# Kernel tuning notes

Hardware: AMD Instinct MI355X
Metric: run time of the kernel (lower is better)

Reference implementation:

```python
import jax, jax.numpy as jnp
import numpy as np

N, E = 50000, 800000
IN_DIM, HID, OUT, HEADS = 128, 128, 64, 4
C1 = HID // HEADS  # 32 per-head channels in gat1
NEG_SLOPE = 0.2


def _gat_conv(x, src, dst, W, a_src, a_dst, b, heads, ch):
    """PyG GATConv (inference): gather -> edge attention -> segment softmax -> scatter."""
    n = x.shape[0]
    h = (x @ W).reshape(n, heads, ch)                      # [N,H,C]
    alpha_src = jnp.einsum('nhc,hc->nh', h, a_src)         # [N,H]
    alpha_dst = jnp.einsum('nhc,hc->nh', h, a_dst)         # [N,H]
    e = jax.nn.leaky_relu(alpha_src[src] + alpha_dst[dst], NEG_SLOPE)  # [E,H]
    m = jax.ops.segment_max(e, dst, num_segments=n)        # per-target max (stable softmax)
    e = jnp.exp(e - m[dst])
    denom = jax.ops.segment_sum(e, dst, num_segments=n)
    alpha = e / (denom[dst] + 1e-16)                       # [E,H]
    out = jax.ops.segment_sum(h[src] * alpha[:, :, None], dst, num_segments=n)  # [N,H,C]
    return out.reshape(n, heads * ch) + b


def setup_inputs() -> dict:
    key = jax.random.key(0)
    ks = jax.random.split(key, 16)
    x = jax.random.normal(ks[0], (N, IN_DIM), dtype=jnp.float32)
    edge_index = jax.random.randint(ks[1], (2, E), 0, N, dtype=jnp.int64)
    s = lambda fan_in: 1.0 / np.sqrt(fan_in)
    return {
        'x': x,
        'edge_index': edge_index,
        'W1': jax.random.normal(ks[2], (IN_DIM, HEADS * C1), jnp.float32) * s(IN_DIM),
        'a_src1': jax.random.normal(ks[3], (HEADS, C1), jnp.float32) * s(C1),
        'a_dst1': jax.random.normal(ks[4], (HEADS, C1), jnp.float32) * s(C1),
        'b1': jnp.zeros((HID,), jnp.float32),
        'W2': jax.random.normal(ks[5], (HID, OUT), jnp.float32) * s(HID),
        'a_src2': jax.random.normal(ks[6], (1, OUT), jnp.float32) * s(OUT),
        'a_dst2': jax.random.normal(ks[7], (1, OUT), jnp.float32) * s(OUT),
        'b2': jnp.zeros((OUT,), jnp.float32),
        'pw1': jax.random.normal(ks[8], (OUT, OUT), jnp.float32) * s(OUT),
        'pb1': jnp.zeros((OUT,), jnp.float32),
        'pw2': jax.random.normal(ks[9], (OUT, OUT), jnp.float32) * s(OUT),
        'pb2': jnp.zeros((OUT,), jnp.float32),
    }


def reference(x, edge_index, W1, a_src1, a_dst1, b1, W2, a_src2, a_dst2, b2, pw1, pb1, pw2, pb2):
    n = x.shape[0]
    # PyG GATConv add_self_loops=True
    loops = jnp.arange(n, dtype=edge_index.dtype)
    src = jnp.concatenate([edge_index[0], loops])
    dst = jnp.concatenate([edge_index[1], loops])
    h = jax.nn.elu(_gat_conv(x, src, dst, W1, a_src1, a_dst1, b1, HEADS, C1))
    h = jax.nn.elu(_gat_conv(h, src, dst, W2, a_src2, a_dst2, b2, 1, OUT))
    # origin_proj: Linear -> ReLU -> Linear
    h = jax.nn.relu(h @ pw1 + pb1)
    return h @ pw2 + pb2
```

## Files before the change

kernel.cpp:

```cpp
#include <hip/hip_runtime.h>
#include <math.h>

#define N_NODES 50000
#define N_EDGES 800000
#define ET (N_EDGES + N_NODES)
#define IN_DIM 128
#define HID 128
#define OUT_DIM 64
#define BW 64
#define NBUCK ((N_NODES + BW - 1) / BW)
#define NBLK 256
#define EPB 3328

typedef __attribute__((ext_vector_type(8))) short bf16x8;
typedef __attribute__((ext_vector_type(4))) float f32x4;

__device__ __forceinline__ float lrelu(float x){ return x >= 0.f ? x : 0.2f * x; }
__device__ __forceinline__ float eluf(float x){ return x > 0.f ? x : expm1f(x); }
__device__ __forceinline__ unsigned f2bf(float f){
    unsigned u = __float_as_uint(f);
    return (u + 0x7fffu + ((u >> 16) & 1u)) >> 16;
}
__device__ __forceinline__ float bflo(unsigned u){ return __uint_as_float(u << 16); }
__device__ __forceinline__ float bfhi(unsigned u){ return __uint_as_float(u & 0xffff0000u); }

__global__ __launch_bounds__(256) void k_count(const int* __restrict__ dst, int* __restrict__ C)
{
    __shared__ int cnt[NBUCK];
    const int tid = threadIdx.x, blk = blockIdx.x;
    for (int i = tid; i < NBUCK; i += 256) cnt[i] = 0;
    __syncthreads();
    #pragma unroll
    for (int j = 0; j < EPB / 256; j++) {
        const int e = blk * EPB + j * 256 + tid;
        if (e < ET) {
            const int d = (e < N_EDGES) ? dst[e] : (e - N_EDGES);
            atomicAdd(&cnt[d >> 6], 1);
        }
    }
    __syncthreads();
    for (int b = tid; b < NBUCK; b += 256) C[b * NBLK + blk] = cnt[b];
}

__global__ __launch_bounds__(256) void k_bsumA(const int* __restrict__ C, int* __restrict__ bsum2)
{
    __shared__ int red[4];
    int v = C[blockIdx.x * NBLK + threadIdx.x];
    #pragma unroll
    for (int off = 32; off > 0; off >>= 1) v += __shfl_down(v, off);
    if ((threadIdx.x & 63) == 0) red[threadIdx.x >> 6] = v;
    __syncthreads();
    if (threadIdx.x == 0) bsum2[blockIdx.x] = red[0] + red[1] + red[2] + red[3];
}

__global__ __launch_bounds__(1024) void k_bscanB(const int* __restrict__ bsum2, int* __restrict__ boff2)
{
    __shared__ int part[1024];
    const int t = threadIdx.x;
    int v = (t < NBUCK) ? bsum2[t] : 0;
    part[t] = v;
    __syncthreads();
    #pragma unroll
    for (int d = 1; d < 1024; d <<= 1) {
        int add = (t >= d) ? part[t - d] : 0;
        __syncthreads();
        part[t] += add;
        __syncthreads();
    }
    if (t < NBUCK) boff2[t] = part[t] - v;
    if (t == 0) boff2[NBUCK] = ET;
}

__global__ __launch_bounds__(256) void k_cscanC(const int* __restrict__ C,
                                                const int* __restrict__ boff2,
                                                int* __restrict__ Cs)
{
    __shared__ int part[256];
    const int t = threadIdx.x, b = blockIdx.x;
    int v = C[b * NBLK + t];
    part[t] = v;
    __syncthreads();
    #pragma unroll
    for (int d = 1; d < 256; d <<= 1) {
        int add = (t >= d) ? part[t - d] : 0;
        __syncthreads();
        part[t] += add;
        __syncthreads();
    }
    Cs[b * NBLK + t] = boff2[b] + part[t] - v;
}

__global__ __launch_bounds__(256) void k_part2(const int* __restrict__ src,
                                               const int* __restrict__ dst,
                                               const int* __restrict__ Cs,
                                               uint2* __restrict__ part)
{
    __shared__ int base[NBUCK];
    __shared__ int cnt[NBUCK];
    const int tid = threadIdx.x, blk = blockIdx.x;
    for (int b = tid; b < NBUCK; b += 256) { base[b] = Cs[b * NBLK + blk]; cnt[b] = 0; }
    __syncthreads();
    #pragma unroll
    for (int j = 0; j < EPB / 256; j++) {
        const int e = blk * EPB + j * 256 + tid;
        if (e < ET) {
            int s, d;
            if (e < N_EDGES) { s = src[e]; d = dst[e]; } else { s = d = e - N_EDGES; }
            const int b = d >> 6;
            const int r = atomicAdd(&cnt[b], 1);
            part[base[b] + r] = make_uint2((unsigned)d, (unsigned)s);
        }
    }
}

__global__ __launch_bounds__(256) void k_scat2(const int* __restrict__ boff2,
                                               const uint2* __restrict__ part,
                                               int* __restrict__ rowptr,
                                               int* __restrict__ csr_src)
{
    __shared__ int cnt64[BW];
    __shared__ int nbase[BW];
    const int b = blockIdx.x, tid = threadIdx.x;
    const int n0 = b * BW;
    const int lo = boff2[b], hi = boff2[b + 1];
    if (tid < BW) cnt64[tid] = 0;
    __syncthreads();
    for (int i = lo + tid; i < hi; i += 256) {
        atomicAdd(&cnt64[part[i].x & (BW - 1)], 1);
    }
    __syncthreads();
    if (tid < BW) {
        int v = cnt64[tid];
        int incl = v;
        #pragma unroll
        for (int off = 1; off < 64; off <<= 1) {
            int t2 = __shfl_up(incl, off);
            if (tid >= off) incl += t2;
        }
        const int excl = incl - v;
        nbase[tid] = excl;
        const int n = n0 + tid;
        if (n < N_NODES) rowptr[n] = lo + excl;
        cnt64[tid] = 0;
    }
    if (b == 0 && tid == 0) rowptr[N_NODES] = ET;
    __syncthreads();
    for (int i = lo + tid; i < hi; i += 256) {
        const uint2 p = part[i];
        const int dn = (int)p.x & (BW - 1);
        const int r = atomicAdd(&cnt64[dn], 1);
        csr_src[lo + nbase[dn] + r] = (int)p.y;
    }
}

__global__ __launch_bounds__(256, 2) void k_gemm1(
    const float* __restrict__ x, const float* __restrict__ W1,
    const float* __restrict__ a_s, const float* __restrict__ a_d,
    unsigned* __restrict__ h1b, float* __restrict__ as1, float* __restrict__ ad1)
{
    __shared__ unsigned sWt[128 * 68];
    __shared__ unsigned sxb[64 * 68];
    const int tid = threadIdx.x;
    const int wave = tid >> 6;
    const int lane = tid & 63;
    const int ll   = lane & 15;
    const int quad = lane >> 4;
    const int n0 = blockIdx.x * 64;

    for (int idx = tid; idx < 8192; idx += 256) {
        const int n = idx & 127, kp = idx >> 7;
        const float w0 = W1[(2 * kp) * 128 + n];
        const float w1 = W1[(2 * kp + 1) * 128 + n];
        sWt[n * 68 + kp] = f2bf(w0) | (f2bf(w1) << 16);
    }
    for (int idx = tid; idx < 4096; idx += 256) {
        const int node = idx >> 6, kp = idx & 63;
        const int n = n0 + node;
        unsigned pk = 0;
        if (n < N_NODES) {
            const float x0 = x[n * 128 + 2 * kp];
            const float x1 = x[n * 128 + 2 * kp + 1];
            pk = f2bf(x0) | (f2bf(x1) << 16);
        }
        sxb[node * 68 + kp] = pk;
    }
    __syncthreads();

    f32x4 acc[8];
    #pragma unroll
    for (int t = 0; t < 8; t++) acc[t] = (f32x4){0.f, 0.f, 0.f, 0.f};

    #pragma unroll
    for (int kk = 0; kk < 4; kk++) {
        const int kpo = 16 * kk + 4 * quad;
        const bf16x8 a = *(const bf16x8*)&sxb[(16 * wave + ll) * 68 + kpo];
        #pragma unroll
        for (int t = 0; t < 8; t++) {
            const bf16x8 b = *(const bf16x8*)&sWt[(16 * t + ll) * 68 + kpo];
            acc[t] = __builtin_amdgcn_mfma_f32_16x16x32_bf16(a, b, acc[t], 0, 0, 0);
        }
    }

    float as_v[8], ad_v[8];
    #pragma unroll
    for (int t = 0; t < 8; t++) { as_v[t] = a_s[16 * t + ll]; ad_v[t] = a_d[16 * t + ll]; }
    unsigned short* h1u = (unsigned short*)h1b;
    #pragma unroll
    for (int r = 0; r < 4; r++) {
        const int n = n0 + 16 * wave + 4 * quad + r;
        float ps0 = acc[0][r] * as_v[0] + acc[1][r] * as_v[1];
        float ps1 = acc[2][r] * as_v[2] + acc[3][r] * as_v[3];
        float ps2 = acc[4][r] * as_v[4] + acc[5][r] * as_v[5];
        float ps3 = acc[6][r] * as_v[6] + acc[7][r] * as_v[7];
        float pd0 = acc[0][r] * ad_v[0] + acc[1][r] * ad_v[1];
        float pd1 = acc[2][r] * ad_v[2] + acc[3][r] * ad_v[3];
        float pd2 = acc[4][r] * ad_v[4] + acc[5][r] * ad_v[5];
        float pd3 = acc[6][r] * ad_v[6] + acc[7][r] * ad_v[7];
        #pragma unroll
        for (int off = 1; off < 16; off <<= 1) {
            ps0 += __shfl_xor(ps0, off); ps1 += __shfl_xor(ps1, off);
            ps2 += __shfl_xor(ps2, off); ps3 += __shfl_xor(ps3, off);
            pd0 += __shfl_xor(pd0, off); pd1 += __shfl_xor(pd1, off);
            pd2 += __shfl_xor(pd2, off); pd3 += __shfl_xor(pd3, off);
        }
        if (n < N_NODES) {
            #pragma unroll
            for (int t = 0; t < 8; t++)
                h1u[n * 128 + 16 * t + ll] = (unsigned short)f2bf(acc[t][r]);
            if (ll == 0) {
                as1[n * 4 + 0] = ps0; as1[n * 4 + 1] = ps1;
                as1[n * 4 + 2] = ps2; as1[n * 4 + 3] = ps3;
                ad1[n * 4 + 0] = pd0; ad1[n * 4 + 1] = pd1;
                ad1[n * 4 + 2] = pd2; ad1[n * 4 + 3] = pd3;
            }
        }
    }
}

__global__ __launch_bounds__(256) void k_aggr1(
    const int* __restrict__ rowptr, const int* __restrict__ csr_src,
    const float* __restrict__ as1, const float* __restrict__ ad1,
    const uint4* __restrict__ h1u4, float* __restrict__ acc1)
{
    const int d  = blockIdx.x * 16 + (threadIdx.x >> 4);
    const int c8 = threadIdx.x & 15;
    const int hd = c8 >> 2;
    const int r0 = rowptr[d], r1 = rowptr[d + 1];
    const float adv = ad1[d * 4 + hd];
    float den = 0.f;
    float acc[8];
    #pragma unroll
    for (int m = 0; m < 8; m++) acc[m] = 0.f;
    int i = r0;
    for (; i + 2 <= r1; i += 2) {
        const int s0 = csr_src[i], s1 = csr_src[i + 1];
        const float e0 = as1[s0 * 4 + hd], e1 = as1[s1 * 4 + hd];
        const uint4 u0 = h1u4[s0 * 16 + c8];
        const uint4 u1 = h1u4[s1 * 16 + c8];
        const float w0 = expf(lrelu(e0 + adv));
        const float w1 = expf(lrelu(e1 + adv));
        den += w0 + w1;
        acc[0] = fmaf(bflo(u0.x), w0, acc[0]); acc[1] = fmaf(bfhi(u0.x), w0, acc[1]);
        acc[2] = fmaf(bflo(u0.y), w0, acc[2]); acc[3] = fmaf(bfhi(u0.y), w0, acc[3]);
        acc[4] = fmaf(bflo(u0.z), w0, acc[4]); acc[5] = fmaf(bfhi(u0.z), w0, acc[5]);
        acc[6] = fmaf(bflo(u0.w), w0, acc[6]); acc[7] = fmaf(bfhi(u0.w), w0, acc[7]);
        acc[0] = fmaf(bflo(u1.x), w1, acc[0]); acc[1] = fmaf(bfhi(u1.x), w1, acc[1]);
        acc[2] = fmaf(bflo(u1.y), w1, acc[2]); acc[3] = fmaf(bfhi(u1.y), w1, acc[3]);
        acc[4] = fmaf(bflo(u1.z), w1, acc[4]); acc[5] = fmaf(bfhi(u1.z), w1, acc[5]);
        acc[6] = fmaf(bflo(u1.w), w1, acc[6]); acc[7] = fmaf(bfhi(u1.w), w1, acc[7]);
    }
    if (i < r1) {
        const int s = csr_src[i];
        const float w = expf(lrelu(as1[s * 4 + hd] + adv));
        const uint4 u = h1u4[s * 16 + c8];
        den += w;
        acc[0] = fmaf(bflo(u.x), w, acc[0]); acc[1] = fmaf(bfhi(u.x), w, acc[1]);
        acc[2] = fmaf(bflo(u.y), w, acc[2]); acc[3] = fmaf(bfhi(u.y), w, acc[3]);
        acc[4] = fmaf(bflo(u.z), w, acc[4]); acc[5] = fmaf(bfhi(u.z), w, acc[5]);
        acc[6] = fmaf(bflo(u.w), w, acc[6]); acc[7] = fmaf(bfhi(u.w), w, acc[7]);
    }
    const float inv = 1.f / (den + 1e-16f);
    float4 o0 = make_float4(acc[0] * inv, acc[1] * inv, acc[2] * inv, acc[3] * inv);
    float4 o1 = make_float4(acc[4] * inv, acc[5] * inv, acc[6] * inv, acc[7] * inv);
    ((float4*)acc1)[d * 32 + 2 * c8 + 0] = o0;
    ((float4*)acc1)[d * 32 + 2 * c8 + 1] = o1;
}

__global__ __launch_bounds__(256, 4) void k_layer2(
    const float* __restrict__ acc1, const float* __restrict__ b1,
    const float* __restrict__ W2, const float* __restrict__ a_s2, const float* __restrict__ a_d2,
    unsigned* __restrict__ h2b, float* __restrict__ as2, float* __restrict__ ad2)
{
    __shared__ float sW[32 * 64];
    __shared__ float sx[128 * 32];
    float4* sW4 = (float4*)sW;
    float4* sx4 = (float4*)sx;
    const float4* a14 = (const float4*)acc1;
    const float4* W24 = (const float4*)W2;
    const float4* b14 = (const float4*)b1;
    const int tid = threadIdx.x;
    const int cg = tid & 7;
    const int ng = tid >> 3;
    const int n0 = blockIdx.x * 128;

    float4 acc[4][2];
    #pragma unroll
    for (int m = 0; m < 4; m++) { acc[m][0] = make_float4(0,0,0,0); acc[m][1] = make_float4(0,0,0,0); }

    for (int c = 0; c < 4; c++) {
        __syncthreads();
        #pragma unroll
        for (int j = 0; j < 2; j++) {
            const int idx = tid + 256 * j;
            float4 v = W24[c * 512 + idx];
            const int k = idx >> 4, f = idx & 15;
            sW4[k * 16 + ((f & 1) << 3) + (f >> 1)] = v;
        }
        #pragma unroll
        for (int j = 0; j < 4; j++) {
            const int idx = tid + 256 * j;
            const int node = idx >> 3, q = idx & 7;
            const int n = n0 + node;
            float4 v = make_float4(0,0,0,0);
            if (n < N_NODES) {
                v = a14[n * 32 + c * 8 + q];
                const float4 bb = b14[c * 8 + q];
                v.x = eluf(v.x + bb.x);
                v.y = eluf(v.y + bb.y);
                v.z = eluf(v.z + bb.z);
                v.w = eluf(v.w + bb.w);
            }
            sx4[node * 8 + (q ^ ((node >> 3) & 7))] = v;
        }
        __syncthreads();
        #pragma unroll 2
        for (int k4 = 0; k4 < 8; k4++) {
            float4 w0[4], w1[4];
            #pragma unroll
            for (int ks = 0; ks < 4; ks++) {
                w0[ks] = sW4[(4 * k4 + ks) * 16 + cg];
                w1[ks] = sW4[(4 * k4 + ks) * 16 + 8 + cg];
            }
            float4 xv[4];
            #pragma unroll
            for (int m = 0; m < 4; m++) {
                const int node = 4 * ng + m;
                xv[m] = sx4[node * 8 + (k4 ^ ((node >> 3) & 7))];
            }
            #pragma unroll
            for (int m = 0; m < 4; m++) {
                const float4 xm = xv[m];
                #define FMA8(S, KS) \
                    acc[m][0].x = fmaf(S, w0[KS].x, acc[m][0].x); \
                    acc[m][0].y = fmaf(S, w0[KS].y, acc[m][0].y); \
                    acc[m][0].z = fmaf(S, w0[KS].z, acc[m][0].z); \
                    acc[m][0].w = fmaf(S, w0[KS].w, acc[m][0].w); \
                    acc[m][1].x = fmaf(S, w1[KS].x, acc[m][1].x); \
                    acc[m][1].y = fmaf(S, w1[KS].y, acc[m][1].y); \
                    acc[m][1].z = fmaf(S, w1[KS].z, acc[m][1].z); \
                    acc[m][1].w = fmaf(S, w1[KS].w, acc[m][1].w);
                FMA8(xm.x, 0) FMA8(xm.y, 1) FMA8(xm.z, 2) FMA8(xm.w, 3)
                #undef FMA8
            }
        }
    }

    const float4 as_a = ((const float4*)a_s2)[2 * cg], as_b = ((const float4*)a_s2)[2 * cg + 1];
    const float4 ad_a = ((const float4*)a_d2)[2 * cg], ad_b = ((const float4*)a_d2)[2 * cg + 1];
    #pragma unroll
    for (int m = 0; m < 4; m++) {
        const int n = n0 + 4 * ng + m;
        float ps = acc[m][0].x * as_a.x + acc[m][0].y * as_a.y + acc[m][0].z * as_a.z + acc[m][0].w * as_a.w
                 + acc[m][1].x * as_b.x + acc[m][1].y * as_b.y + acc[m][1].z * as_b.z + acc[m][1].w * as_b.w;
        float pd = acc[m][0].x * ad_a.x + acc[m][0].y * ad_a.y + acc[m][0].z * ad_a.z + acc[m][0].w * ad_a.w
                 + acc[m][1].x * ad_b.x + acc[m][1].y * ad_b.y + acc[m][1].z * ad_b.z + acc[m][1].w * ad_b.w;
        ps += __shfl_xor(ps, 1); ps += __shfl_xor(ps, 2); ps += __shfl_xor(ps, 4);
        pd += __shfl_xor(pd, 1); pd += __shfl_xor(pd, 2); pd += __shfl_xor(pd, 4);
        if (n < N_NODES) {
            uint2 pk;
            pk.x = f2bf(acc[m][0].x) | (f2bf(acc[m][0].y) << 16);
            pk.y = f2bf(acc[m][0].z) | (f2bf(acc[m][0].w) << 16);
            uint2 pk2;
            pk2.x = f2bf(acc[m][1].x) | (f2bf(acc[m][1].y) << 16);
            pk2.y = f2bf(acc[m][1].z) | (f2bf(acc[m][1].w) << 16);
            uint4 pk4 = make_uint4(pk.x, pk.y, pk2.x, pk2.y);
            ((uint4*)h2b)[n * 8 + cg] = pk4;
            if (cg == 0) { as2[n] = ps; ad2[n] = pd; }
        }
    }
}

__global__ __launch_bounds__(256) void k_aggr2(
    const int* __restrict__ rowptr, const int* __restrict__ csr_src,
    const float* __restrict__ as2, const float* __restrict__ ad2,
    const uint4* __restrict__ h2u4, float* __restrict__ acc2)
{
    const int d  = blockIdx.x * 32 + (threadIdx.x >> 3);
    const int c8 = threadIdx.x & 7;
    if (d >= N_NODES) return;
    const int r0 = rowptr[d], r1 = rowptr[d + 1];
    const float adv = ad2[d];
    float den = 0.f;
    float acc[8];
    #pragma unroll
    for (int m = 0; m < 8; m++) acc[m] = 0.f;
    int i = r0;
    for (; i + 2 <= r1; i += 2) {
        const int s0 = csr_src[i], s1 = csr_src[i + 1];
        const float e0 = as2[s0], e1 = as2[s1];
        const uint4 u0 = h2u4[s0 * 8 + c8];
        const uint4 u1 = h2u4[s1 * 8 + c8];
        const float w0 = expf(lrelu(e0 + adv));
        const float w1 = expf(lrelu(e1 + adv));
        den += w0 + w1;
        acc[0] = fmaf(bflo(u0.x), w0, acc[0]); acc[1] = fmaf(bfhi(u0.x), w0, acc[1]);
        acc[2] = fmaf(bflo(u0.y), w0, acc[2]); acc[3] = fmaf(bfhi(u0.y), w0, acc[3]);
        acc[4] = fmaf(bflo(u0.z), w0, acc[4]); acc[5] = fmaf(bfhi(u0.z), w0, acc[5]);
        acc[6] = fmaf(bflo(u0.w), w0, acc[6]); acc[7] = fmaf(bfhi(u0.w), w0, acc[7]);
        acc[0] = fmaf(bflo(u1.x), w1, acc[0]); acc[1] = fmaf(bfhi(u1.x), w1, acc[1]);
        acc[2] = fmaf(bflo(u1.y), w1, acc[2]); acc[3] = fmaf(bfhi(u1.y), w1, acc[3]);
        acc[4] = fmaf(bflo(u1.z), w1, acc[4]); acc[5] = fmaf(bfhi(u1.z), w1, acc[5]);
        acc[6] = fmaf(bflo(u1.w), w1, acc[6]); acc[7] = fmaf(bfhi(u1.w), w1, acc[7]);
    }
    if (i < r1) {
        const int s = csr_src[i];
        const float w = expf(lrelu(as2[s] + adv));
        const uint4 u = h2u4[s * 8 + c8];
        den += w;
        acc[0] = fmaf(bflo(u.x), w, acc[0]); acc[1] = fmaf(bfhi(u.x), w, acc[1]);
        acc[2] = fmaf(bflo(u.y), w, acc[2]); acc[3] = fmaf(bfhi(u.y), w, acc[3]);
        acc[4] = fmaf(bflo(u.z), w, acc[4]); acc[5] = fmaf(bfhi(u.z), w, acc[5]);
        acc[6] = fmaf(bflo(u.w), w, acc[6]); acc[7] = fmaf(bfhi(u.w), w, acc[7]);
    }
    const float inv = 1.f / (den + 1e-16f);
    float4 o0 = make_float4(acc[0] * inv, acc[1] * inv, acc[2] * inv, acc[3] * inv);
    float4 o1 = make_float4(acc[4] * inv, acc[5] * inv, acc[6] * inv, acc[7] * inv);
    ((float4*)acc2)[d * 16 + 2 * c8 + 0] = o0;
    ((float4*)acc2)[d * 16 + 2 * c8 + 1] = o1;
}

__global__ __launch_bounds__(256, 2) void k_out(
    const float* __restrict__ acc2, const float* __restrict__ b2,
    const float* __restrict__ pw1, const float* __restrict__ pb1,
    const float* __restrict__ pw2, const float* __restrict__ pb2,
    float* __restrict__ out)
{
    __shared__ float s1[64 * 64];
    __shared__ float s2[64 * 64];
    __shared__ float so[64][68];
    __shared__ float sp[64][68];
    const int tid = threadIdx.x;
    for (int i = tid; i < 1024; i += 256) {
        ((float4*)s1)[i] = ((const float4*)pw1)[i];
        ((float4*)s2)[i] = ((const float4*)pw2)[i];
    }
    const int cg = tid & 15;
    const int ng = tid >> 4;
    const float4 pb1_4 = ((const float4*)pb1)[cg];
    const float4 pb2_4 = ((const float4*)pb2)[cg];
    const int nGroups = (N_NODES + 63) / 64;
    for (int g = blockIdx.x; g < nGroups; g += gridDim.x) {
        const int n0 = g * 64;
        __syncthreads();
        #pragma unroll
        for (int j = 0; j < 4; j++) {
            const int i = tid + 256 * j;
            const int node = i >> 4, quad = i & 15;
            const int n = n0 + node;
            float4 v = make_float4(0.f, 0.f, 0.f, 0.f);
            if (n < N_NODES) {
                v = ((const float4*)acc2)[n * 16 + quad];
                const float4 bb = ((const float4*)b2)[quad];
                v.x = eluf(v.x + bb.x);
                v.y = eluf(v.y + bb.y);
                v.z = eluf(v.z + bb.z);
                v.w = eluf(v.w + bb.w);
            }
            *(float4*)&so[node][4 * quad] = v;
        }
        __syncthreads();
        float4 p[4];
        #pragma unroll
        for (int m = 0; m < 4; m++) p[m] = pb1_4;
        #pragma unroll 8
        for (int k = 0; k < 64; k++) {
            const float4 w = *(const float4*)&s1[k * 64 + 4 * cg];
            #pragma unroll
            for (int m = 0; m < 4; m++) {
                const float xv = so[4 * ng + m][k];
                p[m].x = fmaf(xv, w.x, p[m].x);
                p[m].y = fmaf(xv, w.y, p[m].y);
                p[m].z = fmaf(xv, w.z, p[m].z);
                p[m].w = fmaf(xv, w.w, p[m].w);
            }
        }
        #pragma unroll
        for (int m = 0; m < 4; m++) {
            p[m].x = fmaxf(p[m].x, 0.f); p[m].y = fmaxf(p[m].y, 0.f);
            p[m].z = fmaxf(p[m].z, 0.f); p[m].w = fmaxf(p[m].w, 0.f);
            *(float4*)&sp[4 * ng + m][4 * cg] = p[m];
        }
        __syncthreads();
        float4 o[4];
        #pragma unroll
        for (int m = 0; m < 4; m++) o[m] = pb2_4;
        #pragma unroll 8
        for (int k = 0; k < 64; k++) {
            const float4 w = *(const float4*)&s2[k * 64 + 4 * cg];
            #pragma unroll
            for (int m = 0; m < 4; m++) {
                const float xv = sp[4 * ng + m][k];
                o[m].x = fmaf(xv, w.x, o[m].x);
                o[m].y = fmaf(xv, w.y, o[m].y);
                o[m].z = fmaf(xv, w.z, o[m].z);
                o[m].w = fmaf(xv, w.w, o[m].w);
            }
        }
        #pragma unroll
        for (int m = 0; m < 4; m++) {
            const int n = n0 + 4 * ng + m;
            if (n < N_NODES) ((float4*)out)[n * 16 + cg] = o[m];
        }
    }
}

extern "C" void kernel_launch(void* const* d_in, const int* in_sizes, int n_in,
                              void* d_out, int out_size, void* d_ws, size_t ws_size,
                              hipStream_t stream)
{
    const float* x      = (const float*)d_in[0];
    const int*   ei     = (const int*)d_in[1];
    const int*   src    = ei;
    const int*   dst    = ei + N_EDGES;
    const float* W1     = (const float*)d_in[2];
    const float* a_src1 = (const float*)d_in[3];
    const float* a_dst1 = (const float*)d_in[4];
    const float* b1     = (const float*)d_in[5];
    const float* W2     = (const float*)d_in[6];
    const float* a_src2 = (const float*)d_in[7];
    const float* a_dst2 = (const float*)d_in[8];
    const float* b2     = (const float*)d_in[9];
    const float* pw1    = (const float*)d_in[10];
    const float* pb1    = (const float*)d_in[11];
    const float* pw2    = (const float*)d_in[12];
    const float* pb2    = (const float*)d_in[13];

    uint2* part  = (uint2*)d_ws;
    int* ibase   = (int*)(part + ET);
    int* rowptr  = ibase;
    int* C       = rowptr + 50001;
    int* Cs      = C + 200192;
    int* bsum2   = Cs + 200192;
    int* boff2   = bsum2 + 782;
    int* csr_src = boff2 + 785;
    unsigned* h1b = (unsigned*)(csr_src + 850000);
    unsigned* h2b = h1b + 3200000;
    float* fws   = (float*)(h2b + 1600000);
    float* as1   = fws;
    float* ad1   = as1 + 200000;
    float* acc1  = ad1 + 200000;
    float* as2   = acc1 + 6400000;
    float* ad2   = as2 + 50000;
    float* acc2  = ad2 + 50000;

    k_count<<<NBLK, 256, 0, stream>>>(dst, C);
    k_bsumA<<<NBUCK, 256, 0, stream>>>(C, bsum2);
    k_bscanB<<<1, 1024, 0, stream>>>(bsum2, boff2);
    k_cscanC<<<NBUCK, 256, 0, stream>>>(C, boff2, Cs);
    k_part2<<<NBLK, 256, 0, stream>>>(src, dst, Cs, part);
    k_scat2<<<NBUCK, 256, 0, stream>>>(boff2, part, rowptr, csr_src);

    k_gemm1<<<(N_NODES + 63) / 64, 256, 0, stream>>>(x, W1, a_src1, a_dst1, h1b, as1, ad1);
    k_aggr1<<<N_NODES / 16, 256, 0, stream>>>(rowptr, csr_src, as1, ad1,
                                              (const uint4*)h1b, acc1);

    k_layer2<<<(N_NODES + 127) / 128, 256, 0, stream>>>(acc1, b1, W2, a_src2, a_dst2, h2b, as2, ad2);
    k_aggr2<<<(N_NODES + 31) / 32, 256, 0, stream>>>(rowptr, csr_src, as2, ad2,
                                                     (const uint4*)h2b, acc2);

    k_out<<<782, 256, 0, stream>>>(acc2, b2, pw1, pb1, pw2, pb2, (float*)d_out);
}
```

Baseline: 258.6 us.

## Rewrite layer-2 GEMM with bf16 MFMA instead of fp32 FMA

The k_layer2 dense projection (ELU(acc1+b1) @ W2) moves from scalar fp32 FMAs to the 16x16x32 bf16 MFMA instruction. Inputs and weights are packed to bf16 in padded LDS tiles, each block handles 64 nodes, and the attention dot products are reduced with 16-lane shuffles. This trades fp32 precision in the GEMM inputs for matrix-core throughput. The output store becomes scattered 16-bit writes instead of 16-byte vector stores.

```diff
diff --git a/kernel.cpp b/kernel.cpp
--- a/kernel.cpp
+++ b/kernel.cpp
@@ -291,101 +291,70 @@
     const float* __restrict__ W2, const float* __restrict__ a_s2, const float* __restrict__ a_d2,
     unsigned* __restrict__ h2b, float* __restrict__ as2, float* __restrict__ ad2)
 {
-    __shared__ float sW[32 * 64];
-    __shared__ float sx[128 * 32];
-    float4* sW4 = (float4*)sW;
-    float4* sx4 = (float4*)sx;
-    const float4* a14 = (const float4*)acc1;
-    const float4* W24 = (const float4*)W2;
-    const float4* b14 = (const float4*)b1;
+    __shared__ unsigned sWt[64 * 68];
+    __shared__ unsigned sxb[64 * 68];
     const int tid = threadIdx.x;
-    const int cg = tid & 7;
-    const int ng = tid >> 3;
-    const int n0 = blockIdx.x * 128;
-
-    float4 acc[4][2];
-    #pragma unroll
-    for (int m = 0; m < 4; m++) { acc[m][0] = make_float4(0,0,0,0); acc[m][1] = make_float4(0,0,0,0); }
-
-    for (int c = 0; c < 4; c++) {
-        __syncthreads();
-        #pragma unroll
-        for (int j = 0; j < 2; j++) {
-            const int idx = tid + 256 * j;
-            float4 v = W24[c * 512 + idx];
-            const int k = idx >> 4, f = idx & 15;
-            sW4[k * 16 + ((f & 1) << 3) + (f >> 1)] = v;
-        }
-        #pragma unroll
-        for (int j = 0; j < 4; j++) {
-            const int idx = tid + 256 * j;
-            const int node = idx >> 3, q = idx & 7;
-            const int n = n0 + node;
-            float4 v = make_float4(0,0,0,0);
-            if (n < N_NODES) {
-                v = a14[n * 32 + c * 8 + q];
-                const float4 bb = b14[c * 8 + q];
-                v.x = eluf(v.x + bb.x);
-                v.y = eluf(v.y + bb.y);
-                v.z = eluf(v.z + bb.z);
-                v.w = eluf(v.w + bb.w);
-            }
-            sx4[node * 8 + (q ^ ((node >> 3) & 7))] = v;
-        }
-        __syncthreads();
-        #pragma unroll 2
-        for (int k4 = 0; k4 < 8; k4++) {
-            float4 w0[4], w1[4];
+    const int wave = tid >> 6;
+    const int lane = tid & 63;
+    const int ll   = lane & 15;
+    const int quad = lane >> 4;
+    const int n0 = blockIdx.x * 64;
+
+    for (int idx = tid; idx < 4096; idx += 256) {
+        const int n = idx & 63, kp = idx >> 6;
+        const float w0 = W2[(2 * kp) * 64 + n];
+        const float w1 = W2[(2 * kp + 1) * 64 + n];
+        sWt[n * 68 + kp] = f2bf(w0) | (f2bf(w1) << 16);
+    }
+    for (int idx = tid; idx < 4096; idx += 256) {
+        const int node = idx >> 6, kp = idx & 63;
+        const int n = n0 + node;
+        unsigned pk = 0;
+        if (n < N_NODES) {
+            const float v0 = eluf(acc1[n * 128 + 2 * kp]     + b1[2 * kp]);
+            const float v1 = eluf(acc1[n * 128 + 2 * kp + 1] + b1[2 * kp + 1]);
+            pk = f2bf(v0) | (f2bf(v1) << 16);
+        }
+        sxb[node * 68 + kp] = pk;
+    }
+    __syncthreads();
+
+    f32x4 acc[4];
+    #pragma unroll
+    for (int t = 0; t < 4; t++) acc[t] = (f32x4){0.f, 0.f, 0.f, 0.f};
+
+    #pragma unroll
+    for (int kk = 0; kk < 4; kk++) {
+        const int kpo = 16 * kk + 4 * quad;
+        const bf16x8 a = *(const bf16x8*)&sxb[(16 * wave + ll) * 68 + kpo];
+        #pragma unroll
+        for (int t = 0; t < 4; t++) {
+            const bf16x8 b = *(const bf16x8*)&sWt[(16 * t + ll) * 68 + kpo];
+            acc[t] = __builtin_amdgcn_mfma_f32_16x16x32_bf16(a, b, acc[t], 0, 0, 0);
+        }
+    }
+
+    float as_v[4], ad_v[4];
+    #pragma unroll
+    for (int t = 0; t < 4; t++) { as_v[t] = a_s2[16 * t + ll]; ad_v[t] = a_d2[16 * t + ll]; }
+    unsigned short* h2u = (unsigned short*)h2b;
+    #pragma unroll
+    for (int r = 0; r < 4; r++) {
+        const int n = n0 + 16 * wave + 4 * quad + r;
+        float ps = acc[0][r] * as_v[0] + acc[1][r] * as_v[1]
+                 + acc[2][r] * as_v[2] + acc[3][r] * as_v[3];
+        float pd = acc[0][r] * ad_v[0] + acc[1][r] * ad_v[1]
+                 + acc[2][r] * ad_v[2] + acc[3][r] * ad_v[3];
+        #pragma unroll
+        for (int off = 1; off < 16; off <<= 1) {
+            ps += __shfl_xor(ps, off);
+            pd += __shfl_xor(pd, off);
+        }
+        if (n < N_NODES) {
             #pragma unroll
-            for (int ks = 0; ks < 4; ks++) {
-                w0[ks] = sW4[(4 * k4 + ks) * 16 + cg];
-                w1[ks] = sW4[(4 * k4 + ks) * 16 + 8 + cg];
-            }
-            float4 xv[4];
-            #pragma unroll
-            for (int m = 0; m < 4; m++) {
-                const int node = 4 * ng + m;
-                xv[m] = sx4[node * 8 + (k4 ^ ((node >> 3) & 7))];
-            }
-            #pragma unroll
-            for (int m = 0; m < 4; m++) {
-                const float4 xm = xv[m];
-                #define FMA8(S, KS) \
-                    acc[m][0].x = fmaf(S, w0[KS].x, acc[m][0].x); \
-                    acc[m][0].y = fmaf(S, w0[KS].y, acc[m][0].y); \
-                    acc[m][0].z = fmaf(S, w0[KS].z, acc[m][0].z); \
-                    acc[m][0].w = fmaf(S, w0[KS].w, acc[m][0].w); \
-                    acc[m][1].x = fmaf(S, w1[KS].x, acc[m][1].x); \
-                    acc[m][1].y = fmaf(S, w1[KS].y, acc[m][1].y); \
-                    acc[m][1].z = fmaf(S, w1[KS].z, acc[m][1].z); \
-                    acc[m][1].w = fmaf(S, w1[KS].w, acc[m][1].w);
-                FMA8(xm.x, 0) FMA8(xm.y, 1) FMA8(xm.z, 2) FMA8(xm.w, 3)
-                #undef FMA8
-            }
-        }
-    }
-
-    const float4 as_a = ((const float4*)a_s2)[2 * cg], as_b = ((const float4*)a_s2)[2 * cg + 1];
-    const float4 ad_a = ((const float4*)a_d2)[2 * cg], ad_b = ((const float4*)a_d2)[2 * cg + 1];
-    #pragma unroll
-    for (int m = 0; m < 4; m++) {
-        const int n = n0 + 4 * ng + m;
-        float ps = acc[m][0].x * as_a.x + acc[m][0].y * as_a.y + acc[m][0].z * as_a.z + acc[m][0].w * as_a.w
-                 + acc[m][1].x * as_b.x + acc[m][1].y * as_b.y + acc[m][1].z * as_b.z + acc[m][1].w * as_b.w;
-        float pd = acc[m][0].x * ad_a.x + acc[m][0].y * ad_a.y + acc[m][0].z * ad_a.z + acc[m][0].w * ad_a.w
-                 + acc[m][1].x * ad_b.x + acc[m][1].y * ad_b.y + acc[m][1].z * ad_b.z + acc[m][1].w * ad_b.w;
-        ps += __shfl_xor(ps, 1); ps += __shfl_xor(ps, 2); ps += __shfl_xor(ps, 4);
-        pd += __shfl_xor(pd, 1); pd += __shfl_xor(pd, 2); pd += __shfl_xor(pd, 4);
-        if (n < N_NODES) {
-            uint2 pk;
-            pk.x = f2bf(acc[m][0].x) | (f2bf(acc[m][0].y) << 16);
-            pk.y = f2bf(acc[m][0].z) | (f2bf(acc[m][0].w) << 16);
-            uint2 pk2;
-            pk2.x = f2bf(acc[m][1].x) | (f2bf(acc[m][1].y) << 16);
-            pk2.y = f2bf(acc[m][1].z) | (f2bf(acc[m][1].w) << 16);
-            uint4 pk4 = make_uint4(pk.x, pk.y, pk2.x, pk2.y);
-            ((uint4*)h2b)[n * 8 + cg] = pk4;
-            if (cg == 0) { as2[n] = ps; ad2[n] = pd; }
+            for (int t = 0; t < 4; t++)
+                h2u[n * 64 + 16 * t + ll] = (unsigned short)f2bf(acc[t][r]);
+            if (ll == 0) { as2[n] = ps; ad2[n] = pd; }
         }
     }
 }
@@ -574,7 +543,7 @@
     k_aggr1<<<N_NODES / 16, 256, 0, stream>>>(rowptr, csr_src, as1, ad1,
                                               (const uint4*)h1b, acc1);
 
-    k_layer2<<<(N_NODES + 127) / 128, 256, 0, stream>>>(acc1, b1, W2, a_src2, a_dst2, h2b, as2, ad2);
+    k_layer2<<<(N_NODES + 63) / 64, 256, 0, stream>>>(acc1, b1, W2, a_src2, a_dst2, h2b, as2, ad2);
     k_aggr2<<<(N_NODES + 31) / 32, 256, 0, stream>>>(rowptr, csr_src, as2, ad2,
                                                      (const uint4*)h2b, acc2);
 
```

Result: faster. 247.2 us (median of 2 runs) (-4.4%).
